# Kernel tuning notes

Measured on AMD Instinct MI355X. Metric: run time of the kernel, lower is better.

## Reference

```python
import jax, jax.numpy as jnp
import numpy as np

N = 1048576
N_GRID = 256
DX = 1.0 / N_GRID
INV_DX = float(N_GRID)
DT = 2e-5
P_VOL = (DX * 0.5) ** 2
P_RHO = 1.0
P_MASS = P_VOL * P_RHO
E_MOD = 1000.0
NU = 0.2
MU_0 = E_MOD / (2.0 * (1.0 + NU))
LAM_0 = E_MOD * NU / ((1.0 + NU) * (1.0 - 2.0 * NU))
GRAVITY = 50.0


def setup_inputs() -> dict:
    key = jax.random.key(0)
    k = jax.random.split(key, 5)
    x = 0.1 + 0.8 * jax.random.uniform(k[0], (N, 2), dtype=jnp.float32)
    v = 0.1 * jax.random.normal(k[1], (N, 2), dtype=jnp.float32)
    C = 0.5 * jax.random.normal(k[2], (N, 2, 2), dtype=jnp.float32)
    F = jnp.eye(2, dtype=jnp.float32)[None] + 0.1 * jax.random.normal(k[3], (N, 2, 2), dtype=jnp.float32)
    material = jax.random.randint(k[4], (N,), 0, 3, dtype=jnp.int32)
    Jp = jnp.ones((N,), dtype=jnp.float32)
    return {"x": x, "v": v, "C": C, "F": F, "material": material, "Jp": Jp}


def reference(x, v, C, F, material, Jp):
    dt, inv_dx, dx = DT, INV_DX, DX
    base = jnp.floor(x * inv_dx - 0.5).astype(jnp.int32)          # [N,2]
    fx = x * inv_dx - base.astype(x.dtype)                        # [N,2]
    # quadratic B-spline weights, stacked over the 3 taps -> [3,N,2]
    w = jnp.stack([0.5 * (1.5 - fx) ** 2,
                   0.75 - (fx - 1.0) ** 2,
                   0.5 * (fx - 0.5) ** 2], axis=0)

    # deformation gradient update
    F = F + dt * jnp.einsum('nij,njk->nik', C, F)

    h = jnp.exp(10.0 * (1.0 - Jp))
    h = jnp.where(material == 1, 0.3, h)
    mu = jnp.where(material == 0, 0.0, MU_0 * h)
    lam = LAM_0 * h

    # per-particle 2x2 SVD (original pads to 3x3 and slices back)
    U, sig, Vh = jnp.linalg.svd(F)

    # snow plasticity: clamp singular values, track Jp
    clamped = jnp.clip(sig, 1.0 - 2.5e-2, 1.0 + 4.5e-3)
    is_snow = material == 2
    Jp = jnp.where(is_snow, Jp * jnp.prod(sig / clamped, axis=-1), Jp)
    sig = jnp.where(is_snow[:, None], clamped, sig)

    J = jnp.prod(sig, axis=-1)
    eye2 = jnp.eye(2, dtype=x.dtype)
    F_fluid = eye2[None] * jnp.sqrt(J)[:, None, None]             # J^(1/n_dim), n_dim=2
    F_snow = jnp.einsum('nij,nj,njk->nik', U, sig, Vh)
    F = jnp.where((material == 0)[:, None, None], F_fluid,
                  jnp.where(is_snow[:, None, None], F_snow, F))

    R = jnp.einsum('nij,njk->nik', U, Vh)
    stress = (2.0 * mu[:, None, None] * jnp.einsum('nij,nkj->nik', F - R, F)
              + eye2[None] * (lam * J * (J - 1.0))[:, None, None])
    stress = (-dt * P_VOL * 4.0 * inv_dx ** 2) * stress
    affine = stress + P_MASS * C                                   # [N,2,2]

    # ---- P2G scatter over the 3x3 stencil (vectorized over 9 taps) ----
    offs = jnp.array([[i, j] for i in range(3) for j in range(3)], dtype=jnp.int32)  # [9,2]
    weight = w[offs[:, 0], :, 0] * w[offs[:, 1], :, 1]             # [9,N]
    target = base[None, :, :] + offs[:, None, :]                   # [9,N,2]
    idx = target[..., 0] * N_GRID + target[..., 1]                 # [9,N]
    flat_idx = idx.reshape(-1)
    NG2 = N_GRID * N_GRID

    v_add = P_MASS * v - jnp.einsum('nij,nj->ni', affine, x)       # [N,2]
    grid_v = jax.ops.segment_sum((weight[..., None] * v_add[None]).reshape(-1, 2),
                                 flat_idx, num_segments=NG2).reshape(N_GRID, N_GRID, 2)
    grid_affine = jax.ops.segment_sum((weight[..., None, None] * affine[None]).reshape(-1, 4),
                                      flat_idx, num_segments=NG2).reshape(N_GRID, N_GRID, 2, 2)
    grid_m = jax.ops.segment_sum((weight * P_MASS).reshape(-1),
                                 flat_idx, num_segments=NG2).reshape(N_GRID, N_GRID)

    grid_x = jnp.stack(jnp.meshgrid(jnp.arange(N_GRID), jnp.arange(N_GRID), indexing='ij'),
                       axis=-1).astype(x.dtype) * dx               # [G,G,2]
    grid_v = grid_v + jnp.einsum('abij,abj->abi', grid_affine, grid_x)

    # grid ops: momentum -> velocity, gravity, boundary clamps
    m = grid_m[..., None]
    grid_v = jnp.where(m > 0, grid_v / jnp.maximum(m, 1e-12), grid_v)
    grid_v = grid_v.at[:, :, 1].add(-dt * GRAVITY)
    grid_v = grid_v.at[:3, :, 0].max(0.0)
    grid_v = grid_v.at[-2:, :, 0].min(0.0)
    grid_v = grid_v.at[:, :3, 1].max(0.0)
    grid_v = grid_v.at[:, -2:, 1].min(0.0)

    # ---- G2P gather ----
    gvf = grid_v.reshape(NG2, 2)
    g_v = gvf[idx]                                                 # [9,N,2]
    new_v = jnp.sum(weight[..., None] * g_v, axis=0)               # [N,2]
    pos = target.astype(x.dtype) * dx                              # [9,N,2]
    new_C = jnp.sum(weight[..., None, None] * g_v[..., :, None] * pos[..., None, :], axis=0)
    new_C = (new_C - new_v[..., None] * x[:, None, :]) * (4.0 * inv_dx ** 2)

    x = x + dt * new_v
    return (x, new_v, new_C, F, material, Jp)
```

## Files before the change

### kernel.cpp

```cpp
#include <hip/hip_runtime.h>

#define NG 256
#define NG2 (NG*NG)

constexpr float DX      = 1.0f / 256.0f;
constexpr float INV_DX  = 256.0f;
constexpr float DT      = 2e-5f;
constexpr float P_VOL   = (1.0f/512.0f) * (1.0f/512.0f);
constexpr float P_MASS  = P_VOL;
constexpr float MU_0    = 1000.0f / (2.0f * 1.2f);
constexpr float LAM_0   = 1000.0f * 0.2f / (1.2f * 0.6f);
constexpr float GRAV    = 50.0f;

__device__ __forceinline__ int bin_of(float px, float py) {
    int bx = (int)floorf(px * INV_DX - 0.5f);
    int by = (int)floorf(py * INV_DX - 0.5f);
    bx = min(max(bx, 0), NG - 1);
    by = min(max(by, 0), NG - 1);
    return (bx << 8) | by;
}

__device__ __forceinline__ float bw(float t) {
    float at = fabsf(t);
    float a  = fmaxf(1.5f - at, 0.0f);
    float w1 = 0.75f - t * t;
    float w2 = 0.5f * a * a;
    return (at < 0.5f) ? w1 : w2;
}


__global__ __launch_bounds__(256) void binrank_kernel(
    const float* __restrict__ x, int* __restrict__ counts, int* __restrict__ rank, int n)
{
    int i = blockIdx.x * blockDim.x + threadIdx.x;
    if (i >= n) return;
    float2 p = ((const float2*)x)[i];
    int b = bin_of(p.x, p.y);
    rank[i] = atomicAdd(&counts[b], 1);
}

__global__ __launch_bounds__(256) void scan1_kernel(
    const int* __restrict__ counts, int* __restrict__ starts, int* __restrict__ bsum)
{
    __shared__ int tmp[256];
    int t = threadIdx.x, b = blockIdx.x;
    int v = counts[b * 256 + t];
    tmp[t] = v;
    __syncthreads();
    #pragma unroll
    for (int off = 1; off < 256; off <<= 1) {
        int add = (t >= off) ? tmp[t - off] : 0;
        __syncthreads();
        tmp[t] += add;
        __syncthreads();
    }
    starts[b * 256 + t] = tmp[t] - v;
    if (t == 255) bsum[b] = tmp[255];
}

__global__ __launch_bounds__(256) void scan2_kernel(int* __restrict__ bsum)
{
    __shared__ int tmp[256];
    int t = threadIdx.x;
    int v = bsum[t];
    tmp[t] = v;
    __syncthreads();
    #pragma unroll
    for (int off = 1; off < 256; off <<= 1) {
        int add = (t >= off) ? tmp[t - off] : 0;
        __syncthreads();
        tmp[t] += add;
        __syncthreads();
    }
    bsum[t] = tmp[t] - v;
}

__global__ __launch_bounds__(256) void scan3_kernel(
    int* __restrict__ starts, const int* __restrict__ bsum, int n)
{
    int i = blockIdx.x * blockDim.x + threadIdx.x;
    if (i < NG2) starts[i] += bsum[i >> 8];
    if (i == 0) starts[NG2] = n;
}


__global__ __launch_bounds__(256) void compute_scatter_kernel(
    const float* __restrict__ x, const float* __restrict__ v,
    const float* __restrict__ C, const float* __restrict__ F,
    const int* __restrict__ mat, const float* __restrict__ Jp,
    const int* __restrict__ starts, const int* __restrict__ rank,
    float4* __restrict__ srec,
    float4* __restrict__ F_out4, float* __restrict__ mat_out, float* __restrict__ Jp_out,
    int n)
{
    int i = blockIdx.x * blockDim.x + threadIdx.x;
    if (i >= n) return;

    float2 xp = ((const float2*)x)[i];
    float2 vp = ((const float2*)v)[i];
    float4 Cp = ((const float4*)C)[i];
    float4 Fp = ((const float4*)F)[i];
    int    m  = mat[i];
    float  jp = Jp[i];

    float px = xp.x, py = xp.y;
    float C00 = Cp.x, C01 = Cp.y, C10 = Cp.z, C11 = Cp.w;
    float a = Fp.x, b = Fp.y, c = Fp.z, d = Fp.w;

    float na = a + DT*(C00*a + C01*c);
    float nb = b + DT*(C00*b + C01*d);
    float nc = c + DT*(C10*a + C11*c);
    float nd = d + DT*(C10*b + C11*d);
    a = na; b = nb; c = nc; d = nd;

    float h = expf(10.0f * (1.0f - jp));
    if (m == 1) h = 0.3f;
    float mu  = (m == 0) ? 0.0f : MU_0 * h;
    float lam = LAM_0 * h;

    float S00 = a*a + c*c, S01 = a*b + c*d, S11 = b*b + d*d;
    float mh = 0.5f*(S00 + S11), dh = 0.5f*(S00 - S11);
    float delta = sqrtf(dh*dh + S01*S01);
    float sig1 = sqrtf(fmaxf(mh + delta, 0.0f));
    float sig2 = sqrtf(fmaxf(mh - delta, 0.0f));
    float e0, e1;
    if (dh >= 0.0f) { e0 = delta + dh; e1 = S01; }
    else            { e0 = S01;        e1 = delta - dh; }
    float elen = sqrtf(e0*e0 + e1*e1);
    float vc, vs;
    if (elen > 1e-30f) { float il = 1.0f/elen; vc = e0*il; vs = e1*il; }
    else               { vc = 1.0f; vs = 0.0f; }
    float inv1 = 1.0f / fmaxf(sig1, 1e-30f);
    float inv2 = 1.0f / fmaxf(sig2, 1e-30f);
    float u1x = ( a*vc + b*vs) * inv1, u1y = ( c*vc + d*vs) * inv1;
    float u2x = (-a*vs + b*vc) * inv2, u2y = (-c*vs + d*vc) * inv2;

    if (m == 2) {
        float c1 = fminf(fmaxf(sig1, 1.0f - 2.5e-2f), 1.0f + 4.5e-3f);
        float c2 = fminf(fmaxf(sig2, 1.0f - 2.5e-2f), 1.0f + 4.5e-3f);
        jp = jp * (sig1 / c1) * (sig2 / c2);
        sig1 = c1; sig2 = c2;
    }
    float J = sig1 * sig2;

    if (m == 0) {
        float s = sqrtf(J);
        a = s; b = 0.0f; c = 0.0f; d = s;
    } else if (m == 2) {
        a = sig1*u1x*vc - sig2*u2x*vs;
        b = sig1*u1x*vs + sig2*u2x*vc;
        c = sig1*u1y*vc - sig2*u2y*vs;
        d = sig1*u1y*vs + sig2*u2y*vc;
    }
    float R00 = u1x*vc - u2x*vs, R01 = u1x*vs + u2x*vc;
    float R10 = u1y*vc - u2y*vs, R11 = u1y*vs + u2y*vc;

    float k2mu = 2.0f * mu;
    float fr00 = a - R00, fr01 = b - R01, fr10 = c - R10, fr11 = d - R11;
    float ljj  = lam * J * (J - 1.0f);
    float st00 = k2mu*(fr00*a + fr01*b) + ljj;
    float st01 = k2mu*(fr00*c + fr01*d);
    float st10 = k2mu*(fr10*a + fr11*b);
    float st11 = k2mu*(fr10*c + fr11*d) + ljj;
    const float coef = -DT * P_VOL * 4.0f * INV_DX * INV_DX;
    float A00 = coef*st00 + P_MASS*C00;
    float A01 = coef*st01 + P_MASS*C01;
    float A10 = coef*st10 + P_MASS*C10;
    float A11 = coef*st11 + P_MASS*C11;

    float bx_ = P_MASS*vp.x - (A00*px + A01*py);
    float by_ = P_MASS*vp.y - (A10*px + A11*py);

    int sidx = starts[bin_of(px, py)] + rank[i];
    srec[2*sidx]     = make_float4(px * INV_DX, py * INV_DX, bx_, by_);
    srec[2*sidx + 1] = make_float4(A00, A01, A10, A11);

    F_out4[i]  = make_float4(a, b, c, d);
    mat_out[i] = (float)m;
    Jp_out[i]  = jp;
}

__global__ __launch_bounds__(256) void gather_grid_kernel(
    const float4* __restrict__ srec, const int* __restrict__ starts,
    float2* __restrict__ gv)
{
    int bid  = blockIdx.x;
    int swz  = (bid & 7) * (4096 / 8) + (bid >> 3);
    int gtid  = swz * 256 + threadIdx.x;
    int cell  = gtid >> 4;
    int slice = gtid & 15;
    int gi = cell >> 8, gj = cell & (NG - 1);

    float fgi = (float)gi, fgj = (float)gj;
    float posx = fgi * DX, posy = fgj * DX;
    float msum = 0.0f, mvx = 0.0f, mvy = 0.0f;

    int j0 = max(gj - 2, 0);

    int sArr[3], eArr[3];
    #pragma unroll
    for (int t3 = 0; t3 < 3; ++t3) {
        int bi = gi - 2 + t3;
        bool valid = (bi >= 0);
        int row = (valid ? bi : 0) << 8;
        sArr[t3] = valid ? starts[row + j0] : 0;
        eArr[t3] = valid ? starts[row + gj + 1] : 0;
    }

    #pragma unroll
    for (int t3 = 0; t3 < 3; ++t3) {
        int s = sArr[t3], e = eArr[t3];
        for (int k = s + slice; k < e; k += 16) {
            float4 r0 = srec[2*k];
            float4 r1 = srec[2*k + 1];
            float w = bw(r0.x - fgi) * bw(r0.y - fgj);
            msum += w;
            mvx  += w * (r0.z + r1.x * posx + r1.y * posy);
            mvy  += w * (r0.w + r1.z * posx + r1.w * posy);
        }
    }

    #pragma unroll
    for (int off = 1; off < 16; off <<= 1) {
        msum += __shfl_xor(msum, off);
        mvx  += __shfl_xor(mvx,  off);
        mvy  += __shfl_xor(mvy,  off);
    }

    if (slice == 0) {
        float mass = msum * P_MASS;
        float vx = mvx, vy = mvy;
        if (mass > 0.0f) {
            float im = 1.0f / fmaxf(mass, 1e-12f);
            vx *= im; vy *= im;
        }
        vy -= DT * GRAV;
        if (gi < 3)      vx = fmaxf(vx, 0.0f);
        if (gi >= NG-2)  vx = fminf(vx, 0.0f);
        if (gj < 3)      vy = fmaxf(vy, 0.0f);
        if (gj >= NG-2)  vy = fminf(vy, 0.0f);
        gv[cell] = make_float2(vx, vy);
    }
}

__global__ __launch_bounds__(256) void g2p_kernel(
    const float* __restrict__ x, const float2* __restrict__ gv,
    float* __restrict__ x_out, float* __restrict__ v_out, float* __restrict__ C_out,
    int n)
{
    int i = blockIdx.x * blockDim.x + threadIdx.x;
    if (i >= n) return;

    float2 xp = ((const float2*)x)[i];
    float px = xp.x, py = xp.y;
    float bxf = floorf(px * INV_DX - 0.5f), byf = floorf(py * INV_DX - 0.5f);
    float fx = px * INV_DX - bxf, fy = py * INV_DX - byf;
    float wxs[3] = { 0.5f*(1.5f-fx)*(1.5f-fx), 0.75f-(fx-1.0f)*(fx-1.0f), 0.5f*(fx-0.5f)*(fx-0.5f) };
    float wys[3] = { 0.5f*(1.5f-fy)*(1.5f-fy), 0.75f-(fy-1.0f)*(fy-1.0f), 0.5f*(fy-0.5f)*(fy-0.5f) };
    int bix = (int)bxf, biy = (int)byf;

    float nvx = 0.0f, nvy = 0.0f;
    float c00 = 0.0f, c01 = 0.0f, c10 = 0.0f, c11 = 0.0f;
    #pragma unroll
    for (int ii = 0; ii < 3; ++ii) {
        float posx = (bxf + (float)ii) * DX;
        int rowbase = (bix + ii) * NG + biy;
        #pragma unroll
        for (int jj = 0; jj < 3; ++jj) {
            float w = wxs[ii] * wys[jj];
            float posy = (byf + (float)jj) * DX;
            float2 g = gv[rowbase + jj];
            nvx += w * g.x; nvy += w * g.y;
            c00 += w * g.x * posx; c01 += w * g.x * posy;
            c10 += w * g.y * posx; c11 += w * g.y * posy;
        }
    }
    const float K = 4.0f * INV_DX * INV_DX;
    c00 = (c00 - nvx * px) * K; c01 = (c01 - nvx * py) * K;
    c10 = (c10 - nvy * px) * K; c11 = (c11 - nvy * py) * K;

    ((float2*)x_out)[i] = make_float2(px + DT * nvx, py + DT * nvy);
    ((float2*)v_out)[i] = make_float2(nvx, nvy);
    ((float4*)C_out)[i] = make_float4(c00, c01, c10, c11);
}

extern "C" void kernel_launch(void* const* d_in, const int* in_sizes, int n_in,
                              void* d_out, int out_size, void* d_ws, size_t ws_size,
                              hipStream_t stream) {
    const float* x   = (const float*)d_in[0];
    const float* v   = (const float*)d_in[1];
    const float* C   = (const float*)d_in[2];
    const float* F   = (const float*)d_in[3];
    const int*   mat = (const int*)d_in[4];
    const float* Jp  = (const float*)d_in[5];

    int n = in_sizes[0] / 2;

    float* out     = (float*)d_out;
    float* x_out   = out;
    float* v_out   = out + (size_t)2*n;
    float* C_out   = out + (size_t)4*n;
    float* F_out   = out + (size_t)8*n;
    float* mat_out = out + (size_t)12*n;
    float* Jp_out  = out + (size_t)13*n;

    int blocks = (n + 255) / 256;

    char* ws = (char*)d_ws;
    size_t off = 0;
    int* counts = (int*)(ws + off); off += (size_t)NG2 * 4;
    int* starts = (int*)(ws + off); off += (size_t)(NG2 + 1) * 4;
    int* bsum   = (int*)(ws + off); off += 256 * 4;
    int* rank   = (int*)(ws + off); off += (size_t)n * 4;
    off = (off + 63) & ~(size_t)63;
    float4* srec = (float4*)(ws + off); off += (size_t)n * 32;
    float2* gv   = (float2*)(ws + off); off += (size_t)NG2 * 8;

    hipMemsetAsync(counts, 0, (size_t)NG2 * 4, stream);
    binrank_kernel<<<blocks, 256, 0, stream>>>(x, counts, rank, n);
    scan1_kernel<<<NG2/256, 256, 0, stream>>>(counts, starts, bsum);
    scan2_kernel<<<1, 256, 0, stream>>>(bsum);
    scan3_kernel<<<NG2/256, 256, 0, stream>>>(starts, bsum, n);
    compute_scatter_kernel<<<blocks, 256, 0, stream>>>(x, v, C, F, mat, Jp,
                                                       starts, rank, srec,
                                                       (float4*)F_out, mat_out, Jp_out, n);
    gather_grid_kernel<<<(NG2*16)/256, 256, 0, stream>>>(srec, starts, gv);
    g2p_kernel<<<blocks, 256, 0, stream>>>(x, gv, x_out, v_out, C_out, n);
}
```

Measured before the change: 130.0 us.

## Replicate bin counters across eight slots and place sorted records in output buffer

The per-cell particle counters are split into 8 replicas chosen by thread block, which spreads atomic increments across more addresses. The counters are laid out interleaved as bin-major then replica, so a single prefix scan still yields contiguous per-bin ranges that the gather kernel can use unchanged. The scan grows eightfold and the second scan level now handles 2048 partial sums. The sorted particle records are also written into the not-yet-used x/v/C region of the output buffer instead of a separate workspace allocation.

After: 134.5 us. 1.03x slower.

```diff
diff --git a/kernel.cpp b/kernel.cpp
--- a/kernel.cpp
+++ b/kernel.cpp
@@ -2,6 +2,7 @@
 
 #define NG 256
 #define NG2 (NG*NG)
+#define NREP 8
 
 constexpr float DX      = 1.0f / 256.0f;
 constexpr float INV_DX  = 256.0f;
@@ -36,15 +37,17 @@
     if (i >= n) return;
     float2 p = ((const float2*)x)[i];
     int b = bin_of(p.x, p.y);
-    rank[i] = atomicAdd(&counts[b], 1);
+    int rep = (i >> 8) & (NREP - 1);
+    rank[i] = atomicAdd(&counts[rep * NG2 + b], 1);
 }
 
 __global__ __launch_bounds__(256) void scan1_kernel(
-    const int* __restrict__ counts, int* __restrict__ starts, int* __restrict__ bsum)
+    const int* __restrict__ counts, int* __restrict__ starts8, int* __restrict__ bsum)
 {
     __shared__ int tmp[256];
-    int t = threadIdx.x, b = blockIdx.x;
-    int v = counts[b * 256 + t];
+    int t = threadIdx.x, blk = blockIdx.x;
+    int f = blk * 256 + t;
+    int v = counts[(f & (NREP-1)) * NG2 + (f >> 3)];
     tmp[t] = v;
     __syncthreads();
     #pragma unroll
@@ -54,33 +57,38 @@
         tmp[t] += add;
         __syncthreads();
     }
-    starts[b * 256 + t] = tmp[t] - v;
-    if (t == 255) bsum[b] = tmp[255];
+    starts8[f] = tmp[t] - v;
+    if (t == 255) bsum[blk] = tmp[255];
 }
 
 __global__ __launch_bounds__(256) void scan2_kernel(int* __restrict__ bsum)
 {
-    __shared__ int tmp[256];
+    __shared__ int tsum[256];
     int t = threadIdx.x;
-    int v = bsum[t];
-    tmp[t] = v;
+    int loc[8];
+    int s = 0;
+    #pragma unroll
+    for (int k = 0; k < 8; ++k) { loc[k] = bsum[t * 8 + k]; s += loc[k]; }
+    tsum[t] = s;
     __syncthreads();
     #pragma unroll
     for (int off = 1; off < 256; off <<= 1) {
-        int add = (t >= off) ? tmp[t - off] : 0;
+        int add = (t >= off) ? tsum[t - off] : 0;
         __syncthreads();
-        tmp[t] += add;
+        tsum[t] += add;
         __syncthreads();
     }
-    bsum[t] = tmp[t] - v;
+    int run = tsum[t] - s;
+    #pragma unroll
+    for (int k = 0; k < 8; ++k) { int v = loc[k]; bsum[t * 8 + k] = run; run += v; }
 }
 
 __global__ __launch_bounds__(256) void scan3_kernel(
-    int* __restrict__ starts, const int* __restrict__ bsum, int n)
-{
-    int i = blockIdx.x * blockDim.x + threadIdx.x;
-    if (i < NG2) starts[i] += bsum[i >> 8];
-    if (i == 0) starts[NG2] = n;
+    int* __restrict__ starts8, const int* __restrict__ bsum, int n)
+{
+    int f = blockIdx.x * blockDim.x + threadIdx.x;
+    starts8[f] += bsum[f >> 8];
+    if (f == 0) starts8[NG2 * NREP] = n;
 }
 
 
@@ -88,7 +96,7 @@
     const float* __restrict__ x, const float* __restrict__ v,
     const float* __restrict__ C, const float* __restrict__ F,
     const int* __restrict__ mat, const float* __restrict__ Jp,
-    const int* __restrict__ starts, const int* __restrict__ rank,
+    const int* __restrict__ starts8, const int* __restrict__ rank,
     float4* __restrict__ srec,
     float4* __restrict__ F_out4, float* __restrict__ mat_out, float* __restrict__ Jp_out,
     int n)
@@ -171,7 +179,8 @@
     float bx_ = P_MASS*vp.x - (A00*px + A01*py);
     float by_ = P_MASS*vp.y - (A10*px + A11*py);
 
-    int sidx = starts[bin_of(px, py)] + rank[i];
+    int rep  = (i >> 8) & (NREP - 1);
+    int sidx = starts8[bin_of(px, py) * NREP + rep] + rank[i];
     srec[2*sidx]     = make_float4(px * INV_DX, py * INV_DX, bx_, by_);
     srec[2*sidx + 1] = make_float4(A00, A01, A10, A11);
 
@@ -181,7 +190,7 @@
 }
 
 __global__ __launch_bounds__(256) void gather_grid_kernel(
-    const float4* __restrict__ srec, const int* __restrict__ starts,
+    const float4* __restrict__ srec, const int* __restrict__ starts8,
     float2* __restrict__ gv)
 {
     int bid  = blockIdx.x;
@@ -203,8 +212,8 @@
         int bi = gi - 2 + t3;
         bool valid = (bi >= 0);
         int row = (valid ? bi : 0) << 8;
-        sArr[t3] = valid ? starts[row + j0] : 0;
-        eArr[t3] = valid ? starts[row + gj + 1] : 0;
+        sArr[t3] = valid ? starts8[(row + j0) * NREP] : 0;
+        eArr[t3] = valid ? starts8[(row + gj + 1) * NREP] : 0;
     }
 
     #pragma unroll
@@ -304,26 +313,27 @@
     float* mat_out = out + (size_t)12*n;
     float* Jp_out  = out + (size_t)13*n;
 
+    float4* srec = (float4*)out;
+
     int blocks = (n + 255) / 256;
 
     char* ws = (char*)d_ws;
     size_t off = 0;
-    int* counts = (int*)(ws + off); off += (size_t)NG2 * 4;
-    int* starts = (int*)(ws + off); off += (size_t)(NG2 + 1) * 4;
-    int* bsum   = (int*)(ws + off); off += 256 * 4;
-    int* rank   = (int*)(ws + off); off += (size_t)n * 4;
+    int* counts  = (int*)(ws + off); off += (size_t)NG2 * NREP * 4;
+    int* starts8 = (int*)(ws + off); off += ((size_t)NG2 * NREP + 1) * 4;
+    int* bsum    = (int*)(ws + off); off += 2048 * 4;
+    int* rank    = (int*)(ws + off); off += (size_t)n * 4;
     off = (off + 63) & ~(size_t)63;
-    float4* srec = (float4*)(ws + off); off += (size_t)n * 32;
     float2* gv   = (float2*)(ws + off); off += (size_t)NG2 * 8;
 
-    hipMemsetAsync(counts, 0, (size_t)NG2 * 4, stream);
+    hipMemsetAsync(counts, 0, (size_t)NG2 * NREP * 4, stream);
     binrank_kernel<<<blocks, 256, 0, stream>>>(x, counts, rank, n);
-    scan1_kernel<<<NG2/256, 256, 0, stream>>>(counts, starts, bsum);
+    scan1_kernel<<<(NG2*NREP)/256, 256, 0, stream>>>(counts, starts8, bsum);
     scan2_kernel<<<1, 256, 0, stream>>>(bsum);
-    scan3_kernel<<<NG2/256, 256, 0, stream>>>(starts, bsum, n);
+    scan3_kernel<<<(NG2*NREP)/256, 256, 0, stream>>>(starts8, bsum, n);
     compute_scatter_kernel<<<blocks, 256, 0, stream>>>(x, v, C, F, mat, Jp,
-                                                       starts, rank, srec,
+                                                       starts8, rank, srec,
                                                        (float4*)F_out, mat_out, Jp_out, n);
-    gather_grid_kernel<<<(NG2*16)/256, 256, 0, stream>>>(srec, starts, gv);
+    gather_grid_kernel<<<(NG2*16)/256, 256, 0, stream>>>(srec, starts8, gv);
     g2p_kernel<<<blocks, 256, 0, stream>>>(x, gv, x_out, v_out, C_out, n);
 }
```
